# Kernel tuning notes

Hardware: AMD Instinct MI355X
Metric: run time of the kernel (lower is better)

The kernel has to match this reference:

```python
import jax, jax.numpy as jnp
import numpy as np

HIDDEN = 1024
NUM_HEADS = 16
HEAD_SIZE = HIDDEN // NUM_HEADS
B, S = 2, 2048


def setup_inputs() -> dict:
    key = jax.random.key(0)
    k_x, k_wqkv, k_bqkv, k_wo, k_bo = jax.random.split(key, 5)
    x = jax.random.normal(k_x, (B, S, HIDDEN), dtype=jnp.float32)
    # Dense kernels, fan-in scaled like lecun_normal init
    Wqkv = jax.random.normal(k_wqkv, (HIDDEN, 3 * HIDDEN), dtype=jnp.float32) / np.sqrt(HIDDEN)
    bqkv = jnp.zeros((3 * HIDDEN,), dtype=jnp.float32)
    Wo = jax.random.normal(k_wo, (HIDDEN, HIDDEN), dtype=jnp.float32) / np.sqrt(HIDDEN)
    bo = jnp.zeros((HIDDEN,), dtype=jnp.float32)
    return {"x": x, "Wqkv": Wqkv, "bqkv": bqkv, "Wo": Wo, "bo": bo}


def reference(x, Wqkv, bqkv, Wo, bo):
    b, s, h = x.shape
    qkv = jnp.einsum('bsh,hf->bsf', x, Wqkv) + bqkv          # [b, s, 3*h]
    qkv = qkv.reshape(b, s, 3, NUM_HEADS, HEAD_SIZE)
    q, k, v = qkv[:, :, 0], qkv[:, :, 1], qkv[:, :, 2]        # [b, s, nh, hd]
    scale = 1.0 / np.sqrt(HEAD_SIZE)
    scores = jnp.einsum('bqhd,bkhd->bhqk', q, k) * scale      # [b, nh, s, s]
    weights = jax.nn.softmax(scores, axis=-1)
    attn = jnp.einsum('bhqk,bkhd->bqhd', weights, v)          # [b, s, nh, hd]
    attn = attn.reshape(b, s, h)
    return jnp.einsum('bsh,hf->bsf', attn, Wo) + bo
```

## Files before the change

kernel.cpp:

```cpp
#include <hip/hip_runtime.h>
#include <hip/hip_bf16.h>

#define HIDDEN 1024
#define NH 16
#define BATCH 2
#define SEQ 2048

typedef __attribute__((ext_vector_type(8))) short bf16x8;
typedef __attribute__((ext_vector_type(4))) float f32x4;
typedef __attribute__((ext_vector_type(2))) uint uint2v;

__device__ __forceinline__ ushort f2bf(float f) {
    __hip_bfloat16 h = __float2bfloat16(f);
    return *reinterpret_cast<ushort*>(&h);
}
__device__ __forceinline__ float fexp2(float x) {
#if __has_builtin(__builtin_amdgcn_exp2f)
    return __builtin_amdgcn_exp2f(x);
#else
    return exp2f(x);
#endif
}
__device__ __forceinline__ uint pack_bf_trunc(float a, float b) {
    return __builtin_amdgcn_perm(__float_as_uint(b), __float_as_uint(a), 0x07060302u);
}

__device__ __forceinline__ void bfly(uint &a, uint &b) {
#if __has_builtin(__builtin_amdgcn_permlane16_swap)
    uint2v t = __builtin_amdgcn_permlane16_swap(a, b, false, false);
    uint2v s = __builtin_amdgcn_permlane32_swap(t[0], t[1], false, false);
    a = s[0]; b = s[1];
#else
    asm volatile("v_permlane16_swap_b32 %0, %1" : "+v"(a), "+v"(b));
    asm volatile("v_permlane32_swap_b32 %0, %1" : "+v"(a), "+v"(b));
#endif
}

__device__ __forceinline__ void async_copy16(const ushort* g, ushort* l) {
    __builtin_amdgcn_global_load_lds((const __attribute__((address_space(1))) void*)g,
                                     (__attribute__((address_space(3))) void*)l,
                                     16, 0, 0);
}

__global__ void prep_kernel(const float* __restrict__ x,
                            const float* __restrict__ Wqkv,
                            const float* __restrict__ Wo,
                            ushort* __restrict__ xb,
                            ushort* __restrict__ Wt,
                            ushort* __restrict__ WoT)
{
    __shared__ float t[32][33];
    const int bid = blockIdx.x;
    const int tid = threadIdx.x;

    if (bid < 4096) {
        int i = (bid * 256 + tid) * 4;
        float4 v = *(const float4*)(x + i);
        ushort4 w;
        w.x = f2bf(v.x); w.y = f2bf(v.y); w.z = f2bf(v.z); w.w = f2bf(v.w);
        *(ushort4*)(xb + i) = w;
        return;
    }
    const int r = tid >> 3;
    const int c = (tid & 7) * 4;
    if (bid < 7168) {
        int tt = bid - 4096;
        int k0 = (tt & 31) * 32;
        int n0 = (tt >> 5) * 32;
        const int N = 3 * HIDDEN, K = HIDDEN;
        float4 v = *(const float4*)(Wqkv + (size_t)(k0 + r) * N + n0 + c);
        t[r][c] = v.x; t[r][c + 1] = v.y; t[r][c + 2] = v.z; t[r][c + 3] = v.w;
        __syncthreads();
        ushort4 w;
        w.x = f2bf(t[c + 0][r]); w.y = f2bf(t[c + 1][r]);
        w.z = f2bf(t[c + 2][r]); w.w = f2bf(t[c + 3][r]);
        *(ushort4*)(Wt + (size_t)(n0 + r) * K + k0 + c) = w;
    } else {
        int tt = bid - 7168;
        int k0 = (tt & 31) * 32;
        int n0 = (tt >> 5) * 32;
        const int N = HIDDEN, K = HIDDEN;
        float4 v = *(const float4*)(Wo + (size_t)(k0 + r) * N + n0 + c);
        t[r][c] = v.x; t[r][c + 1] = v.y; t[r][c + 2] = v.z; t[r][c + 3] = v.w;
        __syncthreads();
        ushort4 w;
        w.x = f2bf(t[c + 0][r]); w.y = f2bf(t[c + 1][r]);
        w.z = f2bf(t[c + 2][r]); w.w = f2bf(t[c + 3][r]);
        *(ushort4*)(WoT + (size_t)(n0 + r) * K + k0 + c) = w;
    }
}

__global__ __launch_bounds__(256, 3)
void gemm_mfma_bf16_kernel(const ushort* __restrict__ A,
                           const ushort* __restrict__ Bt,
                           const float* __restrict__ bias,
                           ushort* __restrict__ C, int N,
                           int qscale_cols, float qscale,
                           ushort* __restrict__ vtg, int vt_mode)
{
    constexpr int K = 1024;
    __shared__ ushort As[128 * 64];
    __shared__ ushort Bs[128 * 64];

    const int tid  = threadIdx.x;
    const int wave = tid >> 6;
    const int lane = tid & 63;
    const int l16  = lane & 15;
    const int quad = lane >> 4;
    const int wm = wave & 1, wn = wave >> 1;

    const int bm = blockIdx.y * 128;
    const int bn = blockIdx.x * 128;

    const int srow = lane >> 3;
    const int lblk = (lane & 7) ^ srow;
    const ushort* Ag = A  + (size_t)(bm + wave * 32 + srow) * K + lblk * 8;
    const ushort* Bg = Bt + (size_t)(bn + wave * 32 + srow) * K + lblk * 8;
    ushort* Asl = As + wave * 32 * 64;
    ushort* Bsl = Bs + wave * 32 * 64;

    f32x4 acc[4][4];
    #pragma unroll
    for (int i = 0; i < 4; i++)
        #pragma unroll
        for (int j = 0; j < 4; j++) acc[i][j] = (f32x4){0.f, 0.f, 0.f, 0.f};

    for (int k0 = 0; k0 < K; k0 += 64) {
        __syncthreads();
        #pragma unroll
        for (int t = 0; t < 4; t++) {
            async_copy16(Ag + (size_t)t * 8 * K + k0, Asl + t * 8 * 64);
            async_copy16(Bg + (size_t)t * 8 * K + k0, Bsl + t * 8 * 64);
        }
        __syncthreads();

        #pragma unroll
        for (int s = 0; s < 2; s++) {
            bf16x8 af[4], bfr[4];
            #pragma unroll
            for (int i = 0; i < 4; i++) {
                int m = wm * 64 + i * 16 + l16;
                int n = wn * 64 + i * 16 + l16;
                af[i]  = *(const bf16x8*)&As[m * 64 + (((s * 4 + quad) ^ (m & 7)) << 3)];
                bfr[i] = *(const bf16x8*)&Bs[n * 64 + (((s * 4 + quad) ^ (n & 7)) << 3)];
            }
            #pragma unroll
            for (int i = 0; i < 4; i++)
                #pragma unroll
                for (int j = 0; j < 4; j++)
                    acc[i][j] = __builtin_amdgcn_mfma_f32_16x16x32_bf16(af[i], bfr[j], acc[i][j], 0, 0, 0);
        }
    }

    #pragma unroll
    for (int j = 0; j < 4; j++) {
        int col = bn + wn * 64 + j * 16 + l16;
        float bv = bias[col];
        if (vt_mode && col >= 2048) {
            int dfull = col - 2048;
            int hh = dfull >> 6, dd = dfull & 63;
            int bb = bm >> 11;
            int sb = ((bm & 2047) + wm * 64) >> 6;
            ushort tmp[16];
            #pragma unroll
            for (int i = 0; i < 4; i++)
                #pragma unroll
                for (int r = 0; r < 4; r++)
                    tmp[r * 4 + i] = f2bf(acc[i][j][r] + bv);
            ushort* dst = vtg + ((size_t)((bb * NH + hh) * 64 + dd)) * SEQ
                          + sb * 64 + quad * 16;
            *(uint4*)dst = *(const uint4*)tmp;
            *(uint4*)(dst + 8) = *(const uint4*)(tmp + 8);
        } else {
            float s = (col < qscale_cols) ? qscale : 1.0f;
            #pragma unroll
            for (int i = 0; i < 4; i++) {
                int row0 = bm + wm * 64 + i * 16 + quad * 4;
                #pragma unroll
                for (int r = 0; r < 4; r++)
                    C[(size_t)(row0 + r) * N + col] = f2bf((acc[i][j][r] + bv) * s);
            }
        }
    }
}

__global__ __launch_bounds__(256, 4)
void gemm_out_kernel(const ushort* __restrict__ A,
                     const ushort* __restrict__ Bt,
                     const float* __restrict__ bias,
                     float* __restrict__ C)
{
    constexpr int K = 1024, N = 1024;
    __shared__ ushort As[128 * 64];
    __shared__ ushort Bs[64 * 64];

    const int tid  = threadIdx.x;
    const int wave = tid >> 6;
    const int lane = tid & 63;
    const int l16  = lane & 15;
    const int quad = lane >> 4;
    const int wm = wave & 1, wn = wave >> 1;

    const int bm = blockIdx.y * 128;
    const int bn = blockIdx.x * 64;

    const int srow = lane >> 3;
    const int lblk = (lane & 7) ^ srow;
    const ushort* Ag = A  + (size_t)(bm + wave * 32 + srow) * K + lblk * 8;
    const ushort* Bg = Bt + (size_t)(bn + wave * 16 + srow) * K + lblk * 8;
    ushort* Asl = As + wave * 32 * 64;
    ushort* Bsl = Bs + wave * 16 * 64;

    f32x4 acc[4][2];
    #pragma unroll
    for (int i = 0; i < 4; i++)
        #pragma unroll
        for (int j = 0; j < 2; j++) acc[i][j] = (f32x4){0.f, 0.f, 0.f, 0.f};

    for (int k0 = 0; k0 < K; k0 += 64) {
        __syncthreads();
        #pragma unroll
        for (int t = 0; t < 4; t++)
            async_copy16(Ag + (size_t)t * 8 * K + k0, Asl + t * 8 * 64);
        #pragma unroll
        for (int t = 0; t < 2; t++)
            async_copy16(Bg + (size_t)t * 8 * K + k0, Bsl + t * 8 * 64);
        __syncthreads();

        #pragma unroll
        for (int s = 0; s < 2; s++) {
            bf16x8 af[4], bfr[2];
            #pragma unroll
            for (int i = 0; i < 4; i++) {
                int m = wm * 64 + i * 16 + l16;
                af[i] = *(const bf16x8*)&As[m * 64 + (((s * 4 + quad) ^ (m & 7)) << 3)];
            }
            #pragma unroll
            for (int j = 0; j < 2; j++) {
                int n = wn * 32 + j * 16 + l16;
                bfr[j] = *(const bf16x8*)&Bs[n * 64 + (((s * 4 + quad) ^ (n & 7)) << 3)];
            }
            #pragma unroll
            for (int i = 0; i < 4; i++)
                #pragma unroll
                for (int j = 0; j < 2; j++)
                    acc[i][j] = __builtin_amdgcn_mfma_f32_16x16x32_bf16(af[i], bfr[j], acc[i][j], 0, 0, 0);
        }
    }

    #pragma unroll
    for (int j = 0; j < 2; j++) {
        int col = bn + wn * 32 + j * 16 + l16;
        float bv = bias[col];
        #pragma unroll
        for (int i = 0; i < 4; i++) {
            int row0 = bm + wm * 64 + i * 16 + quad * 4;
            #pragma unroll
            for (int r = 0; r < 4; r++)
                C[(size_t)(row0 + r) * N + col] = acc[i][j][r] + bv;
        }
    }
}

__device__ __forceinline__ void qk_sub(
    const ushort* Ks, const bf16x8 (&a_q)[2][2], f32x4 (&sc)[2][4],
    int l16, int quad)
{
    #pragma unroll
    for (int nt = 0; nt < 4; nt++) {
        int key = nt * 16 + l16;
        bf16x8 bk0 = *(const bf16x8*)&Ks[key * 64 + ((quad ^ (key & 7)) << 3)];
        bf16x8 bk1 = *(const bf16x8*)&Ks[key * 64 + (((4 + quad) ^ (key & 7)) << 3)];
        #pragma unroll
        for (int mg = 0; mg < 2; mg++) {
            f32x4 a = (f32x4){0.f, 0.f, 0.f, 0.f};
            a = __builtin_amdgcn_mfma_f32_16x16x32_bf16(bk0, a_q[mg][0], a, 0, 0, 0);
            a = __builtin_amdgcn_mfma_f32_16x16x32_bf16(bk1, a_q[mg][1], a, 0, 0, 0);
            sc[mg][nt] = a;
        }
    }
}

__device__ __forceinline__ void sm_sub(const f32x4 (&sc)[2][4], bf16x8 (&ap)[2][2])
{
    #pragma unroll
    for (int mg = 0; mg < 2; mg++) {
        uint w00 = pack_bf_trunc(fexp2(sc[mg][0][0]), fexp2(sc[mg][1][0]));
        uint w01 = pack_bf_trunc(fexp2(sc[mg][0][1]), fexp2(sc[mg][1][1]));
        uint w02 = pack_bf_trunc(fexp2(sc[mg][0][2]), fexp2(sc[mg][1][2]));
        uint w03 = pack_bf_trunc(fexp2(sc[mg][0][3]), fexp2(sc[mg][1][3]));
        uint w10 = pack_bf_trunc(fexp2(sc[mg][2][0]), fexp2(sc[mg][3][0]));
        uint w11 = pack_bf_trunc(fexp2(sc[mg][2][1]), fexp2(sc[mg][3][1]));
        uint w12 = pack_bf_trunc(fexp2(sc[mg][2][2]), fexp2(sc[mg][3][2]));
        uint w13 = pack_bf_trunc(fexp2(sc[mg][2][3]), fexp2(sc[mg][3][3]));
        bfly(w00, w02);
        bfly(w01, w03);
        bfly(w10, w12);
        bfly(w11, w13);
        union { uint u[4]; bf16x8 h; } u0, u1;
        u0.u[0] = w00; u0.u[1] = w10; u0.u[2] = w01; u0.u[3] = w11;
        u1.u[0] = w02; u1.u[1] = w12; u1.u[2] = w03; u1.u[3] = w13;
        ap[mg][0] = u0.h;
        ap[mg][1] = u1.h;
    }
}

__device__ __forceinline__ void pv_sub(
    const ushort* Vs, const bf16x8 (&ap)[2][2], f32x4 (&o)[2][4],
    f32x4 (&lacc)[2], const bf16x8 &b_ones, int l16, int quad)
{
    #pragma unroll
    for (int nt = 0; nt < 4; nt++) {
        int d = nt * 16 + l16;
        bf16x8 bv0 = *(const bf16x8*)&Vs[d * 64 + ((quad ^ (d & 7)) << 3)];
        bf16x8 bv1 = *(const bf16x8*)&Vs[d * 64 + (((4 + quad) ^ (d & 7)) << 3)];
        #pragma unroll
        for (int mg = 0; mg < 2; mg++) {
            o[mg][nt] = __builtin_amdgcn_mfma_f32_16x16x32_bf16(ap[mg][0], bv0, o[mg][nt], 0, 0, 0);
            o[mg][nt] = __builtin_amdgcn_mfma_f32_16x16x32_bf16(ap[mg][1], bv1, o[mg][nt], 0, 0, 0);
        }
    }
    #pragma unroll
    for (int mg = 0; mg < 2; mg++) {
        lacc[mg] = __builtin_amdgcn_mfma_f32_16x16x32_bf16(ap[mg][0], b_ones, lacc[mg], 0, 0, 0);
        lacc[mg] = __builtin_amdgcn_mfma_f32_16x16x32_bf16(ap[mg][1], b_ones, lacc[mg], 0, 0, 0);
    }
}

__global__ __launch_bounds__(256, 2)
void attn_mfma_v14_kernel(const ushort* __restrict__ qkvb,
                          const ushort* __restrict__ vtg,
                          ushort* __restrict__ attn)
{
    __shared__ __align__(16) ushort smem[32768];

    const int tid  = threadIdx.x;
    const int wave = tid >> 6;
    const int lane = tid & 63;
    const int l16  = lane & 15;
    const int quad = lane >> 4;

    const int obid = blockIdx.x;
    const int qb = (obid >> 3) & 15;
    const int bh = (obid & 7) * 4 + (obid >> 7);
    const int h  = bh & (NH - 1);
    const int b  = bh >> 4;

    const int qbase = qb * 128 + wave * 32;
    const int hoff  = h * 64;

    bf16x8 a_q[2][2];
    #pragma unroll
    for (int mg = 0; mg < 2; mg++) {
        int qrow = b * SEQ + qbase + mg * 16 + l16;
        const ushort* qp = qkvb + (size_t)qrow * 3072 + hoff + quad * 8;
        a_q[mg][0] = *(const bf16x8*)qp;
        a_q[mg][1] = *(const bf16x8*)(qp + 32);
    }

    f32x4 o[2][4];
    f32x4 lacc[2];
    #pragma unroll
    for (int mg = 0; mg < 2; mg++) {
        lacc[mg] = (f32x4){0.f, 0.f, 0.f, 0.f};
        #pragma unroll
        for (int nt = 0; nt < 4; nt++) o[mg][nt] = (f32x4){0.f, 0.f, 0.f, 0.f};
    }

    bf16x8 b_ones;
    #pragma unroll
    for (int j = 0; j < 8; j++) b_ones[j] = (short)0x3f80;

    const ushort* kvb    = qkvb + (size_t)b * SEQ * 3072;
    const ushort* vtg_bh = vtg + (size_t)((b * NH + h) * 64) * SEQ;

    const int srow8 = lane >> 3;
    const int gblk  = ((lane & 7) ^ srow8) << 3;
    const ushort* kg = kvb + (size_t)(wave * 16 + srow8) * 3072 + 1024 + hoff + gblk;
    const ushort* vg = vtg_bh + (size_t)(wave * 16 + srow8) * SEQ + gblk;

    ushort* k_dst = smem + wave * 1024;
    ushort* v_dst = smem + 16384 + wave * 1024;

    #pragma unroll
    for (int s = 0; s < 2; s++)
        #pragma unroll
        for (int c = 0; c < 2; c++) {
            async_copy16(kg + (size_t)(s * 64 + c * 8) * 3072,
                         k_dst + s * 4096 + c * 512);
            async_copy16(vg + (size_t)(c * 8) * SEQ + s * 64,
                         v_dst + s * 4096 + c * 512);
        }
    __syncthreads();

    int cur = 0;
    for (int t = 0; t < 16; t++) {
        const int nb = (cur ^ 1) << 13;
        if (t < 15) {
            const int k0n = (t + 1) * 128;
            #pragma unroll
            for (int s = 0; s < 2; s++)
                #pragma unroll
                for (int c = 0; c < 2; c++)
                    async_copy16(kg + (size_t)(k0n + s * 64 + c * 8) * 3072,
                                 k_dst + nb + s * 4096 + c * 512);
        }

        const ushort* Kc = smem + (cur << 13);
        const ushort* Vc = smem + 16384 + (cur << 13);

        f32x4 sc0[2][4], sc1[2][4];
        __builtin_amdgcn_s_setprio(1);
        qk_sub(Kc,        a_q, sc0, l16, quad);
        qk_sub(Kc + 4096, a_q, sc1, l16, quad);
        __builtin_amdgcn_s_setprio(0);

        if (t < 15) {
            const int k0n = (t + 1) * 128;
            #pragma unroll
            for (int s = 0; s < 2; s++)
                #pragma unroll
                for (int c = 0; c < 2; c++)
                    async_copy16(vg + (size_t)(c * 8) * SEQ + k0n + s * 64,
                                 v_dst + nb + s * 4096 + c * 512);
        }

        bf16x8 ap0[2][2];
        sm_sub(sc0, ap0);

        __builtin_amdgcn_s_setprio(1);
        pv_sub(Vc, ap0, o, lacc, b_ones, l16, quad);
        __builtin_amdgcn_s_setprio(0);

        bf16x8 ap1[2][2];
        sm_sub(sc1, ap1);

        __builtin_amdgcn_s_setprio(1);
        pv_sub(Vc + 4096, ap1, o, lacc, b_ones, l16, quad);
        __builtin_amdgcn_s_setprio(0);

        __syncthreads();
        cur ^= 1;
    }

    #pragma unroll
    for (int mg = 0; mg < 2; mg++) {
        #pragma unroll
        for (int r = 0; r < 4; r++) {
            float inv = 1.f / lacc[mg][r];
            int row = b * SEQ + qbase + mg * 16 + quad * 4 + r;
            size_t base = (size_t)row * HIDDEN + hoff + l16;
            #pragma unroll
            for (int nt = 0; nt < 4; nt++)
                attn[base + nt * 16] = f2bf(o[mg][nt][r] * inv);
        }
    }
}

__global__ __launch_bounds__(512, 4)
void attn_mfma_fb_kernel(const ushort* __restrict__ qkvb,
                         ushort* __restrict__ attn)
{
    __shared__ __align__(16) ushort smem[34816];

    const int tid   = threadIdx.x;
    const int wave  = tid >> 6;
    const int wavel = wave & 3;
    const int kh    = wave >> 2;
    const int lane  = tid & 63;
    const int l16   = lane & 15;
    const int quad  = lane >> 4;

    const int qb = blockIdx.x & 15;
    const int bh = blockIdx.x >> 4;
    const int h  = bh & (NH - 1);
    const int b  = bh >> 4;

    const int qbase = qb * 128;
    const int hoff  = h * 64;

    ushort* KsH = smem + kh * 4096;
    ushort* VsH = smem + 8192 + kh * 4096;
    ushort* Psw = smem + 16384 + wave * 2304;

    bf16x8 a_q[2][2];
    #pragma unroll
    for (int mg = 0; mg < 2; mg++) {
        int qrow = b * SEQ + qbase + wavel * 32 + mg * 16 + l16;
        const ushort* qp = qkvb + (size_t)qrow * 3072 + hoff + quad * 8;
        a_q[mg][0] = *(const bf16x8*)qp;
        a_q[mg][1] = *(const bf16x8*)(qp + 32);
    }

    f32x4 o[2][4];
    f32x4 lacc[2];
    #pragma unroll
    for (int mg = 0; mg < 2; mg++) {
        lacc[mg] = (f32x4){0.f, 0.f, 0.f, 0.f};
        #pragma unroll
        for (int nt = 0; nt < 4; nt++) o[mg][nt] = (f32x4){0.f, 0.f, 0.f, 0.f};
    }

    bf16x8 b_ones;
    #pragma unroll
    for (int j = 0; j < 8; j++) b_ones[j] = (short)0x3f80;

    const ushort* kvb = qkvb + (size_t)b * SEQ * 3072;

    for (int t = 0; t < 16; t++) {
        const int k0 = t * 64;
        __syncthreads();
        {
            const int tl = tid & 255;
            #pragma unroll
            for (int i = 0; i < 2; i++) {
                int key = (tl >> 3) + 32 * i;
                int blk = tl & 7;
                const ushort* ksrc = kvb + (size_t)(kh * 1024 + k0 + key) * 3072 + 1024 + hoff + blk * 8;
                uint4 kv = *(const uint4*)ksrc;
                *(uint4*)&KsH[key * 64 + ((blk ^ (key & 7)) << 3)] = kv;
                uint4 vv = *(const uint4*)(ksrc + 1024);
                const ushort* vpp = (const ushort*)&vv;
                int pk_ = (key & 15) * 4 + (key >> 4);
                #pragma unroll
                for (int j = 0; j < 8; j++) {
                    int d = blk * 8 + j;
                    VsH[d * 64 + (((pk_ >> 3) ^ (d & 7)) << 3) + (pk_ & 7)] = vpp[j];
                }
            }
        }
        __syncthreads();

        f32x4 sc[2][4];
        #pragma unroll
        for (int nt = 0; nt < 4; nt++) {
            int key = nt * 16 + l16;
            bf16x8 bk0 = *(const bf16x8*)&KsH[key * 64 + ((quad ^ (key & 7)) << 3)];
            bf16x8 bk1 = *(const bf16x8*)&KsH[key * 64 + (((4 + quad) ^ (key & 7)) << 3)];
            #pragma unroll
            for (int mg = 0; mg < 2; mg++) {
                f32x4 a = (f32x4){0.f, 0.f, 0.f, 0.f};
                a = __builtin_amdgcn_mfma_f32_16x16x32_bf16(a_q[mg][0], bk0, a, 0, 0, 0);
                a = __builtin_amdgcn_mfma_f32_16x16x32_bf16(a_q[mg][1], bk1, a, 0, 0, 0);
                sc[mg][nt] = a;
            }
        }

        #pragma unroll
        for (int mg = 0; mg < 2; mg++) {
            #pragma unroll
            for (int r = 0; r < 4; r++) {
                int q = mg * 16 + quad * 4 + r;
                uint2 pk2;
                pk2.x = pack_bf_trunc(fexp2(sc[mg][0][r]), fexp2(sc[mg][1][r]));
                pk2.y = pack_bf_trunc(fexp2(sc[mg][2][r]), fexp2(sc[mg][3][r]));
                *(uint2*)&Psw[q * 72 + l16 * 4] = pk2;
            }
        }

        asm volatile("s_waitcnt lgkmcnt(0)" ::: "memory");
        bf16x8 a_p[2][2];
        #pragma unroll
        for (int mg = 0; mg < 2; mg++) {
            a_p[mg][0] = *(const bf16x8*)&Psw[(mg * 16 + l16) * 72 + quad * 8];
            a_p[mg][1] = *(const bf16x8*)&Psw[(mg * 16 + l16) * 72 + 32 + quad * 8];
        }

        #pragma unroll
        for (int nt = 0; nt < 4; nt++) {
            int d = nt * 16 + l16;
            bf16x8 bv0 = *(const bf16x8*)&VsH[d * 64 + ((quad ^ (d & 7)) << 3)];
            bf16x8 bv1 = *(const bf16x8*)&VsH[d * 64 + (((4 + quad) ^ (d & 7)) << 3)];
            #pragma unroll
            for (int mg = 0; mg < 2; mg++) {
                o[mg][nt] = __builtin_amdgcn_mfma_f32_16x16x32_bf16(a_p[mg][0], bv0, o[mg][nt], 0, 0, 0);
                o[mg][nt] = __builtin_amdgcn_mfma_f32_16x16x32_bf16(a_p[mg][1], bv1, o[mg][nt], 0, 0, 0);
            }
        }
        #pragma unroll
        for (int mg = 0; mg < 2; mg++) {
            lacc[mg] = __builtin_amdgcn_mfma_f32_16x16x32_bf16(a_p[mg][0], b_ones, lacc[mg], 0, 0, 0);
            lacc[mg] = __builtin_amdgcn_mfma_f32_16x16x32_bf16(a_p[mg][1], b_ones, lacc[mg], 0, 0, 0);
        }
    }

    __syncthreads();
    float* osc = (float*)smem;
    float* lsc = (float*)(smem + 16384);
    const int fo = wavel * 2048 + quad * 64 + l16 * 4;
    const int fl = wavel * 512 + quad * 64 + l16 * 4;
    if (kh == 1) {
        #pragma unroll
        for (int mg = 0; mg < 2; mg++) {
            #pragma unroll
            for (int nt = 0; nt < 4; nt++)
                *(f32x4*)&osc[fo + (mg * 4 + nt) * 256] = o[mg][nt];
            *(f32x4*)&lsc[fl + mg * 256] = lacc[mg];
        }
    }
    __syncthreads();
    if (kh == 0) {
        #pragma unroll
        for (int mg = 0; mg < 2; mg++) {
            #pragma unroll
            for (int nt = 0; nt < 4; nt++)
                o[mg][nt] += *(const f32x4*)&osc[fo + (mg * 4 + nt) * 256];
            lacc[mg] += *(const f32x4*)&lsc[fl + mg * 256];
        }
        #pragma unroll
        for (int mg = 0; mg < 2; mg++) {
            #pragma unroll
            for (int r = 0; r < 4; r++) {
                float inv = 1.f / lacc[mg][r];
                int row = b * SEQ + qbase + wavel * 32 + mg * 16 + quad * 4 + r;
                size_t base = (size_t)row * HIDDEN + hoff + l16;
                #pragma unroll
                for (int nt = 0; nt < 4; nt++)
                    attn[base + nt * 16] = f2bf(o[mg][nt][r] * inv);
            }
        }
    }
}

extern "C" void kernel_launch(void* const* d_in, const int* in_sizes, int n_in,
                              void* d_out, int out_size, void* d_ws, size_t ws_size,
                              hipStream_t stream) {
    const float* x    = (const float*)d_in[0];
    const float* Wqkv = (const float*)d_in[1];
    const float* bqkv = (const float*)d_in[2];
    const float* Wo   = (const float*)d_in[3];
    const float* bo   = (const float*)d_in[4];
    float* out = (float*)d_out;

    const int M = BATCH * SEQ;
    const size_t MB = 1024 * 1024;

    char* ws = (char*)d_ws;
    ushort* qkvb = (ushort*)ws;
    ushort* attn = (ushort*)(ws + 24 * MB);
    ushort* xb   = (ushort*)(ws + 24 * MB);
    ushort* Wt   = (ushort*)(ws + 32 * MB);
    ushort* WoT  = (ushort*)(ws + 38 * MB);
    ushort* vtg  = (ushort*)(ws + 40 * MB);
    const int use_vtg = (ws_size >= 48 * MB) ? 1 : 0;

    const float qscale = 0.125f * 1.44269504088896f;

    prep_kernel<<<8192, 256, 0, stream>>>(x, Wqkv, Wo, xb, Wt, WoT);

    {
        dim3 grid((3 * HIDDEN) / 128, M / 128);
        gemm_mfma_bf16_kernel<<<grid, 256, 0, stream>>>(xb, Wt, bqkv, qkvb,
                                                        3 * HIDDEN, HIDDEN, qscale,
                                                        vtg, use_vtg);
    }

    if (use_vtg) {
        attn_mfma_v14_kernel<<<BATCH * NH * (SEQ / 128), 256, 0, stream>>>(
            qkvb, vtg, attn);
    } else {
        attn_mfma_fb_kernel<<<BATCH * NH * (SEQ / 128), 512, 0, stream>>>(
            qkvb, attn);
    }

    {
        dim3 grid(HIDDEN / 64, M / 128);
        gemm_out_kernel<<<grid, 256, 0, stream>>>(attn, WoT, bo, out);
    }
}
```

Baseline: 174.9 us.

## Add 256x256-tile QKV GEMM with 8 waves and phased async prefetch

```diff
diff --git a/kernel.cpp b/kernel.cpp
--- a/kernel.cpp
+++ b/kernel.cpp
@@ -184,6 +184,171 @@
     }
 }
 
+template<int MH, int NHq, bool RB>
+__device__ __forceinline__ void g1_phase_body(
+    const ushort* Asb, const ushort* Bsb,
+    bf16x8 (&af)[4][2], bf16x8 (&bfr)[2][2],
+    f32x4 (&acc)[2][2][4][2], int l16, int quad, int wmp, int wnp)
+{
+    #pragma unroll
+    for (int ip = 0; ip < 4; ip++) {
+        int m = MH * 128 + wmp * 64 + ip * 16 + l16;
+        #pragma unroll
+        for (int ks = 0; ks < 2; ks++)
+            af[ip][ks] = *(const bf16x8*)&Asb[m * 64 + (((ks * 4 + quad) ^ (m & 7)) << 3)];
+    }
+    if (RB) {
+        #pragma unroll
+        for (int jp = 0; jp < 2; jp++) {
+            int n = NHq * 128 + wnp * 32 + jp * 16 + l16;
+            #pragma unroll
+            for (int ks = 0; ks < 2; ks++)
+                bfr[jp][ks] = *(const bf16x8*)&Bsb[n * 64 + (((ks * 4 + quad) ^ (n & 7)) << 3)];
+        }
+    }
+    __builtin_amdgcn_s_setprio(1);
+    #pragma unroll
+    for (int ip = 0; ip < 4; ip++)
+        #pragma unroll
+        for (int jp = 0; jp < 2; jp++)
+            #pragma unroll
+            for (int ks = 0; ks < 2; ks++)
+                acc[MH][NHq][ip][jp] = __builtin_amdgcn_mfma_f32_16x16x32_bf16(
+                    af[ip][ks], bfr[jp][ks], acc[MH][NHq][ip][jp], 0, 0, 0);
+    __builtin_amdgcn_s_setprio(0);
+}
+
+#define G1_PHASE_SYNC()                                    \
+    asm volatile("s_waitcnt vmcnt(4)" ::: "memory");       \
+    __builtin_amdgcn_s_barrier();                          \
+    asm volatile("" ::: "memory")
+
+__global__ __launch_bounds__(512, 2)
+void gemm1_8p_kernel(const ushort* __restrict__ A,
+                     const ushort* __restrict__ Bt,
+                     const float* __restrict__ bias,
+                     ushort* __restrict__ C,
+                     float qscale,
+                     ushort* __restrict__ vtg)
+{
+    constexpr int Kd = 1024, Nn = 3072;
+    __shared__ __align__(16) ushort smem[65536];
+
+    const int tid  = threadIdx.x;
+    const int lane = tid & 63;
+    const int l16  = lane & 15;
+    const int quad = lane >> 4;
+    const int wv   = tid >> 6;
+    const int wmp  = wv >> 2;
+    const int wnp  = wv & 3;
+
+    const int obid = blockIdx.x;
+    const int wg = (obid & 7) * 24 + (obid >> 3);
+    const int bm = (wg / 12) * 256;
+    const int bn = (wg % 12) * 256;
+
+    const int row0 = tid >> 3;
+    const int blk  = tid & 7;
+    const int swz  = ((blk ^ (row0 & 7)) << 3);
+    const ushort* Ag = A  + (size_t)(bm + row0) * Kd + swz;
+    const ushort* Bg = Bt + (size_t)(bn + row0) * Kd + swz;
+    const int dstT = row0 * 64 + blk * 8;
+
+    auto stageA = [&](int slot, int mh, int kt) {
+        const ushort* s0 = Ag + (size_t)mh * 131072 + (size_t)kt * 64;
+        ushort* d0 = smem + slot * 16384 + mh * 8192 + dstT;
+        async_copy16(s0, d0);
+        async_copy16(s0 + 65536, d0 + 4096);
+    };
+    auto stageB = [&](int slot, int nh, int kt) {
+        const ushort* s0 = Bg + (size_t)nh * 131072 + (size_t)kt * 64;
+        ushort* d0 = smem + 32768 + slot * 16384 + nh * 8192 + dstT;
+        async_copy16(s0, d0);
+        async_copy16(s0 + 65536, d0 + 4096);
+    };
+
+    f32x4 acc[2][2][4][2];
+    #pragma unroll
+    for (int a = 0; a < 2; a++)
+        #pragma unroll
+        for (int b = 0; b < 2; b++)
+            #pragma unroll
+            for (int c = 0; c < 4; c++)
+                #pragma unroll
+                for (int d = 0; d < 2; d++)
+                    acc[a][b][c][d] = (f32x4){0.f, 0.f, 0.f, 0.f};
+
+    stageA(0, 0, 0); stageB(0, 0, 0); stageA(0, 1, 0); stageB(0, 1, 0);
+
+    bf16x8 af[4][2], bfr[2][2];
+
+    #pragma unroll 1
+    for (int t = 0; t < 16; t++) {
+        const int cur = t & 1;
+        const int nxt = cur ^ 1;
+        const ushort* Asb = smem + cur * 16384;
+        const ushort* Bsb = smem + 32768 + cur * 16384;
+        const bool st = (t < 15);
+        const int kt1 = t + 1;
+
+        G1_PHASE_SYNC();
+        if (st) stageA(nxt, 0, kt1);
+        g1_phase_body<0, 0, true>(Asb, Bsb, af, bfr, acc, l16, quad, wmp, wnp);
+
+        G1_PHASE_SYNC();
+        if (st) stageB(nxt, 0, kt1);
+        g1_phase_body<1, 0, false>(Asb, Bsb, af, bfr, acc, l16, quad, wmp, wnp);
+
+        G1_PHASE_SYNC();
+        if (st) stageA(nxt, 1, kt1);
+        g1_phase_body<0, 1, true>(Asb, Bsb, af, bfr, acc, l16, quad, wmp, wnp);
+
+        G1_PHASE_SYNC();
+        if (st) stageB(nxt, 1, kt1);
+        g1_phase_body<1, 1, false>(Asb, Bsb, af, bfr, acc, l16, quad, wmp, wnp);
+    }
+
+    #pragma unroll
+    for (int nh = 0; nh < 2; nh++)
+        #pragma unroll
+        for (int jp = 0; jp < 2; jp++) {
+            int col = bn + nh * 128 + wnp * 32 + jp * 16 + l16;
+            float bv = bias[col];
+            if (col >= 2048) {
+                int dfull = col - 2048;
+                int hh = dfull >> 6, dd = dfull & 63;
+                #pragma unroll
+                for (int mh = 0; mh < 2; mh++) {
+                    int rowchunk = bm + mh * 128 + wmp * 64;
+                    int bb = rowchunk >> 11;
+                    int sb = (rowchunk & 2047) >> 6;
+                    ushort tmp[16];
+                    #pragma unroll
+                    for (int ip = 0; ip < 4; ip++)
+                        #pragma unroll
+                        for (int r = 0; r < 4; r++)
+                            tmp[r * 4 + ip] = f2bf(acc[mh][nh][ip][jp][r] + bv);
+                    ushort* dst = vtg + ((size_t)((bb * NH + hh) * 64 + dd)) * SEQ
+                                  + sb * 64 + quad * 16;
+                    *(uint4*)dst = *(const uint4*)tmp;
+                    *(uint4*)(dst + 8) = *(const uint4*)(tmp + 8);
+                }
+            } else {
+                float s = (col < 1024) ? qscale : 1.0f;
+                #pragma unroll
+                for (int mh = 0; mh < 2; mh++)
+                    #pragma unroll
+                    for (int ip = 0; ip < 4; ip++) {
+                        int r0 = bm + mh * 128 + wmp * 64 + ip * 16 + quad * 4;
+                        #pragma unroll
+                        for (int r = 0; r < 4; r++)
+                            C[(size_t)(r0 + r) * Nn + col] =
+                                f2bf((acc[mh][nh][ip][jp][r] + bv) * s);
+                    }
+            }
+        }
+}
+
 __global__ __launch_bounds__(256, 4)
 void gemm_out_kernel(const ushort* __restrict__ A,
                      const ushort* __restrict__ Bt,
@@ -648,11 +813,13 @@
 
     prep_kernel<<<8192, 256, 0, stream>>>(x, Wqkv, Wo, xb, Wt, WoT);
 
-    {
+    if (use_vtg) {
+        gemm1_8p_kernel<<<192, 512, 0, stream>>>(xb, Wt, bqkv, qkvb, qscale, vtg);
+    } else {
         dim3 grid((3 * HIDDEN) / 128, M / 128);
         gemm_mfma_bf16_kernel<<<grid, 256, 0, stream>>>(xb, Wt, bqkv, qkvb,
                                                         3 * HIDDEN, HIDDEN, qscale,
-                                                        vtg, use_vtg);
+                                                        vtg, 0);
     }
 
     if (use_vtg) {
```

After: 172.5 us. About the same (-1.4%).

## Double-buffer LDS in both projection GEMMs with tile swizzle and MFMA priority

Applied to the files above, without the earlier changes.

```diff
diff --git a/kernel.cpp b/kernel.cpp
--- a/kernel.cpp
+++ b/kernel.cpp
@@ -184,15 +184,17 @@
     }
 }
 
-__global__ __launch_bounds__(256, 4)
-void gemm_out_kernel(const ushort* __restrict__ A,
+__global__ __launch_bounds__(256, 2)
+void gemm1_db_kernel(const ushort* __restrict__ A,
                      const ushort* __restrict__ Bt,
                      const float* __restrict__ bias,
-                     float* __restrict__ C)
-{
-    constexpr int K = 1024, N = 1024;
-    __shared__ ushort As[128 * 64];
-    __shared__ ushort Bs[64 * 64];
+                     ushort* __restrict__ C,
+                     float qscale,
+                     ushort* __restrict__ vtg)
+{
+    constexpr int K = 1024, N = 3072;
+    __shared__ __align__(16) ushort As[2][128 * 64];
+    __shared__ __align__(16) ushort Bs[2][128 * 64];
 
     const int tid  = threadIdx.x;
     const int wave = tid >> 6;
@@ -201,6 +203,113 @@
     const int quad = lane >> 4;
     const int wm = wave & 1, wn = wave >> 1;
 
+    const int obid = blockIdx.x;
+    const int wg = (obid & 7) * 96 + (obid >> 3);
+    const int bm = (wg / 24) * 128;
+    const int bn = (wg % 24) * 128;
+
+    const int srow = lane >> 3;
+    const int lblk = (lane & 7) ^ srow;
+    const ushort* Ag = A  + (size_t)(bm + wave * 32 + srow) * K + lblk * 8;
+    const ushort* Bg = Bt + (size_t)(bn + wave * 32 + srow) * K + lblk * 8;
+
+    auto stage = [&](int slot, int kt) {
+        const int k0 = kt * 64;
+        ushort* Asl = As[slot] + wave * 32 * 64;
+        ushort* Bsl = Bs[slot] + wave * 32 * 64;
+        #pragma unroll
+        for (int t = 0; t < 4; t++) {
+            async_copy16(Ag + (size_t)t * 8 * K + k0, Asl + t * 8 * 64);
+            async_copy16(Bg + (size_t)t * 8 * K + k0, Bsl + t * 8 * 64);
+        }
+    };
+
+    f32x4 acc[4][4];
+    #pragma unroll
+    for (int i = 0; i < 4; i++)
+        #pragma unroll
+        for (int j = 0; j < 4; j++) acc[i][j] = (f32x4){0.f, 0.f, 0.f, 0.f};
+
+    stage(0, 0);
+    __syncthreads();
+
+    for (int t = 0; t < 16; t++) {
+        if (t < 15) stage((t + 1) & 1, t + 1);
+
+        const ushort* Asb = As[t & 1];
+        const ushort* Bsb = Bs[t & 1];
+
+        #pragma unroll
+        for (int s = 0; s < 2; s++) {
+            bf16x8 af[4], bfr[4];
+            #pragma unroll
+            for (int i = 0; i < 4; i++) {
+                int m = wm * 64 + i * 16 + l16;
+                int n = wn * 64 + i * 16 + l16;
+                af[i]  = *(const bf16x8*)&Asb[m * 64 + (((s * 4 + quad) ^ (m & 7)) << 3)];
+                bfr[i] = *(const bf16x8*)&Bsb[n * 64 + (((s * 4 + quad) ^ (n & 7)) << 3)];
+            }
+            __builtin_amdgcn_s_setprio(1);
+            #pragma unroll
+            for (int i = 0; i < 4; i++)
+                #pragma unroll
+                for (int j = 0; j < 4; j++)
+                    acc[i][j] = __builtin_amdgcn_mfma_f32_16x16x32_bf16(af[i], bfr[j], acc[i][j], 0, 0, 0);
+            __builtin_amdgcn_s_setprio(0);
+        }
+
+        __syncthreads();
+    }
+
+    #pragma unroll
+    for (int j = 0; j < 4; j++) {
+        int col = bn + wn * 64 + j * 16 + l16;
+        float bv = bias[col];
+        if (col >= 2048) {
+            int dfull = col - 2048;
+            int hh = dfull >> 6, dd = dfull & 63;
+            int bb = bm >> 11;
+            int sb = ((bm & 2047) + wm * 64) >> 6;
+            ushort tmp[16];
+            #pragma unroll
+            for (int i = 0; i < 4; i++)
+                #pragma unroll
+                for (int r = 0; r < 4; r++)
+                    tmp[r * 4 + i] = f2bf(acc[i][j][r] + bv);
+            ushort* dst = vtg + ((size_t)((bb * NH + hh) * 64 + dd)) * SEQ
+                          + sb * 64 + quad * 16;
+            *(uint4*)dst = *(const uint4*)tmp;
+            *(uint4*)(dst + 8) = *(const uint4*)(tmp + 8);
+        } else {
+            float s = (col < 1024) ? qscale : 1.0f;
+            #pragma unroll
+            for (int i = 0; i < 4; i++) {
+                int row0 = bm + wm * 64 + i * 16 + quad * 4;
+                #pragma unroll
+                for (int r = 0; r < 4; r++)
+                    C[(size_t)(row0 + r) * N + col] = f2bf((acc[i][j][r] + bv) * s);
+            }
+        }
+    }
+}
+
+__global__ __launch_bounds__(256, 3)
+void gemm_out2_kernel(const ushort* __restrict__ A,
+                      const ushort* __restrict__ Bt,
+                      const float* __restrict__ bias,
+                      float* __restrict__ C)
+{
+    constexpr int K = 1024, N = 1024;
+    __shared__ __align__(16) ushort As[2][128 * 64];
+    __shared__ __align__(16) ushort Bs[2][64 * 64];
+
+    const int tid  = threadIdx.x;
+    const int wave = tid >> 6;
+    const int lane = tid & 63;
+    const int l16  = lane & 15;
+    const int quad = lane >> 4;
+    const int wm = wave & 1, wn = wave >> 1;
+
     const int bm = blockIdx.y * 128;
     const int bn = blockIdx.x * 64;
 
@@ -208,24 +317,33 @@
     const int lblk = (lane & 7) ^ srow;
     const ushort* Ag = A  + (size_t)(bm + wave * 32 + srow) * K + lblk * 8;
     const ushort* Bg = Bt + (size_t)(bn + wave * 16 + srow) * K + lblk * 8;
-    ushort* Asl = As + wave * 32 * 64;
-    ushort* Bsl = Bs + wave * 16 * 64;
-
-    f32x4 acc[4][2];
-    #pragma unroll
-    for (int i = 0; i < 4; i++)
-        #pragma unroll
-        for (int j = 0; j < 2; j++) acc[i][j] = (f32x4){0.f, 0.f, 0.f, 0.f};
-
-    for (int k0 = 0; k0 < K; k0 += 64) {
-        __syncthreads();
+
+    auto stage = [&](int slot, int kt) {
+        const int k0 = kt * 64;
+        ushort* Asl = As[slot] + wave * 32 * 64;
+        ushort* Bsl = Bs[slot] + wave * 16 * 64;
         #pragma unroll
         for (int t = 0; t < 4; t++)
             async_copy16(Ag + (size_t)t * 8 * K + k0, Asl + t * 8 * 64);
         #pragma unroll
         for (int t = 0; t < 2; t++)
             async_copy16(Bg + (size_t)t * 8 * K + k0, Bsl + t * 8 * 64);
-        __syncthreads();
+    };
+
+    f32x4 acc[4][2];
+    #pragma unroll
+    for (int i = 0; i < 4; i++)
+        #pragma unroll
+        for (int j = 0; j < 2; j++) acc[i][j] = (f32x4){0.f, 0.f, 0.f, 0.f};
+
+    stage(0, 0);
+    __syncthreads();
+
+    for (int t = 0; t < 16; t++) {
+        if (t < 15) stage((t + 1) & 1, t + 1);
+
+        const ushort* Asb = As[t & 1];
+        const ushort* Bsb = Bs[t & 1];
 
         #pragma unroll
         for (int s = 0; s < 2; s++) {
@@ -233,19 +351,23 @@
             #pragma unroll
             for (int i = 0; i < 4; i++) {
                 int m = wm * 64 + i * 16 + l16;
-                af[i] = *(const bf16x8*)&As[m * 64 + (((s * 4 + quad) ^ (m & 7)) << 3)];
+                af[i] = *(const bf16x8*)&Asb[m * 64 + (((s * 4 + quad) ^ (m & 7)) << 3)];
             }
             #pragma unroll
             for (int j = 0; j < 2; j++) {
                 int n = wn * 32 + j * 16 + l16;
-                bfr[j] = *(const bf16x8*)&Bs[n * 64 + (((s * 4 + quad) ^ (n & 7)) << 3)];
-            }
+                bfr[j] = *(const bf16x8*)&Bsb[n * 64 + (((s * 4 + quad) ^ (n & 7)) << 3)];
+            }
+            __builtin_amdgcn_s_setprio(1);
             #pragma unroll
             for (int i = 0; i < 4; i++)
                 #pragma unroll
                 for (int j = 0; j < 2; j++)
                     acc[i][j] = __builtin_amdgcn_mfma_f32_16x16x32_bf16(af[i], bfr[j], acc[i][j], 0, 0, 0);
-        }
+            __builtin_amdgcn_s_setprio(0);
+        }
+
+        __syncthreads();
     }
 
     #pragma unroll
@@ -648,11 +770,13 @@
 
     prep_kernel<<<8192, 256, 0, stream>>>(x, Wqkv, Wo, xb, Wt, WoT);
 
-    {
+    if (use_vtg) {
+        gemm1_db_kernel<<<768, 256, 0, stream>>>(xb, Wt, bqkv, qkvb, qscale, vtg);
+    } else {
         dim3 grid((3 * HIDDEN) / 128, M / 128);
         gemm_mfma_bf16_kernel<<<grid, 256, 0, stream>>>(xb, Wt, bqkv, qkvb,
                                                         3 * HIDDEN, HIDDEN, qscale,
-                                                        vtg, use_vtg);
+                                                        vtg, 0);
     }
 
     if (use_vtg) {
@@ -665,6 +789,6 @@
 
     {
         dim3 grid(HIDDEN / 64, M / 128);
-        gemm_out_kernel<<<grid, 256, 0, stream>>>(attn, WoT, bo, out);
-    }
-}
+        gemm_out2_kernel<<<grid, 256, 0, stream>>>(attn, WoT, bo, out);
+    }
+}
```

New measurement: 179.7 us. 1.03x slower.
